# Performance work log

Hardware: AMD Instinct MI355X
Metric: run time of the kernel (lower is better)

The kernel has to match this reference:

```python
import jax, jax.numpy as jnp
import numpy as np

NUM_CAPS = 8
NITER = 3
TAU = 1.0
N_NODES = 50000
N_EDGES = 800000
D_FEAT = 128


def _l2norm(v):
    # matches torch fn.normalize(dim=-1, eps=1e-12): v / max(||v||, eps)
    n = jnp.linalg.norm(v, axis=-1, keepdims=True)
    return v / jnp.maximum(n, 1e-12)


def setup_inputs() -> dict:
    key = jax.random.key(0)
    k1, k2, k3 = jax.random.split(key, 3)
    x = jax.random.normal(k1, (N_NODES, D_FEAT), dtype=jnp.float32)
    src = jax.random.randint(k2, (N_EDGES,), 0, N_NODES)
    trg = jax.random.randint(k3, (N_EDGES,), 0, N_NODES)
    edge_index = jnp.stack([src, trg], axis=0).astype(jnp.int64)
    return {"x": x, "edge_index": edge_index}


def reference(x, edge_index):
    num_node, num_dim = x.shape
    dpc = num_dim // NUM_CAPS  # dim per capsule
    src, trg = edge_index[0], edge_index[1]

    xc = _l2norm(x.reshape(num_node, NUM_CAPS, dpc))  # [N, C, d]
    z = xc[src]                                        # [E, C, d] gathered source caps
    u = xc
    for _ in range(NITER):
        # per-edge, per-capsule agreement score
        p = jnp.einsum('ecd,ecd->ec', z, u[trg])       # [E, C]
        p = jax.nn.softmax(p / TAU, axis=1)
        msg = z * p[:, :, None]                        # [E, C, d]
        u = jax.ops.segment_sum(msg, trg, num_segments=num_node)  # [N, C, d]
        u = _l2norm(u + xc)
    return u.reshape(num_node, num_dim)
```

## Files before the change

### kernel.cpp

```cpp
#include <hip/hip_runtime.h>
#include <hip/hip_bf16.h>

#define DF   128
#define DPC  16
#define WPB  4

__device__ __forceinline__ float cap_sum(float v) {
    v += __shfl_xor(v, 1);
    v += __shfl_xor(v, 2);
    v += __shfl_xor(v, 4);
    return v;
}
__device__ __forceinline__ float bits_lo(unsigned int w) {
    union { unsigned int u; float f; } c; c.u = w << 16; return c.f;
}
__device__ __forceinline__ float bits_hi(unsigned int w) {
    union { unsigned int u; float f; } c; c.u = w & 0xFFFF0000u; return c.f;
}
__device__ __forceinline__ unsigned int f2b_pack(float lo, float hi) {
    __hip_bfloat16 a = __float2bfloat16(lo), b = __float2bfloat16(hi);
    unsigned short ua = *reinterpret_cast<unsigned short*>(&a);
    unsigned short ub = *reinterpret_cast<unsigned short*>(&b);
    return ((unsigned int)ub << 16) | ua;
}
__device__ __forceinline__ float2 load_x2(const void* __restrict__ xraw, int fp32,
                                          int node, int lane) {
    size_t off = (size_t)node * DF + (size_t)lane * 2;
    if (fp32) {
        return *reinterpret_cast<const float2*>((const float*)xraw + off);
    } else {
        unsigned int w = ((const unsigned int*)xraw)[(size_t)node * 64 + lane];
        return make_float2(bits_lo(w), bits_hi(w));
    }
}
__device__ __forceinline__ int2 edge_st(const int* __restrict__ ei, int i64,
                                        int e, int n_edges) {
    size_t si = i64 ? (size_t)2 * e             : (size_t)e;
    size_t ti = i64 ? (size_t)2 * (n_edges + e) : (size_t)(n_edges + e);
    return make_int2(ei[si], ei[ti]);
}

__global__ void k_detect_zero(const unsigned int* __restrict__ xw,
                              const unsigned int* __restrict__ ew,
                              int* __restrict__ flags, int* __restrict__ cnt,
                              int n_nodes) {
    if (blockIdx.x == 0) {
        __shared__ int s_nan, s_zero;
        int tid = threadIdx.x;
        if (tid == 0) { s_nan = 0; s_zero = 0; }
        __syncthreads();
        int cnt_nan = 0;
        for (int i = tid; i < 4096; i += 256) {
            unsigned int lo = xw[i] & 0xFFFFu;
            if ((lo & 0x7F80u) == 0x7F80u) cnt_nan++;
        }
        int cnt_zero = 0;
        for (int i = tid; i < 1024; i += 256) {
            if (ew[2 * i + 1] == 0u) cnt_zero++;
        }
        atomicAdd(&s_nan, cnt_nan);
        atomicAdd(&s_zero, cnt_zero);
        __syncthreads();
        if (tid == 0) {
            flags[0] = (s_nan > 0) ? 1 : 0;
            flags[1] = (s_zero > 512) ? 1 : 0;
        }
    } else {
        int i = (blockIdx.x - 1) * 256 + threadIdx.x;
        if (i < n_nodes) cnt[i] = 0;
    }
}

__global__ void k_prep(const void* __restrict__ xraw, unsigned int* __restrict__ xcb,
                       const int* __restrict__ ei, int* __restrict__ cnt,
                       int* __restrict__ elist, const int* __restrict__ flags,
                       int n_nodes, int n_edges, int nb_hist, int K) {
    const int fp32 = flags[0];
    int wid  = (blockIdx.x * blockDim.x + threadIdx.x) >> 6;
    int lane = threadIdx.x & 63;
    if (wid < n_nodes) {
        float2 v = load_x2(xraw, fp32, wid, lane);
        float ss = cap_sum(v.x * v.x + v.y * v.y);
        float scale = 1.0f / fmaxf(sqrtf(ss), 1e-12f);
        xcb[(size_t)wid * 64 + lane] = f2b_pack(v.x * scale, v.y * scale);
    }
    if (blockIdx.x < (unsigned)nb_hist) {
        int e = blockIdx.x * 256 + threadIdx.x;
        if (e < n_edges) {
            int2 st = edge_st(ei, flags[1], e, n_edges);
            if ((unsigned)st.y < (unsigned)n_nodes &&
                (unsigned)st.x < (unsigned)n_nodes) {
                int slot = atomicAdd(&cnt[st.y], 1);
                if (slot < K) elist[st.y * K + slot] = st.x << 8;
            }
        }
    }
}

__global__ void k_route(const int* __restrict__ cnt, const int* __restrict__ elist,
                        const unsigned int* __restrict__ xcb,
                        const void* __restrict__ xraw, const int* __restrict__ flags,
                        float* __restrict__ u_out, int n_nodes, int K) {
    int t    = (blockIdx.x * blockDim.x + threadIdx.x) >> 6;
    int lane = threadIdx.x & 63;
    if (t >= n_nodes) return;
    const int e8 = lane >> 3;
    const int c  = lane & 7;
    const int fp32 = flags[0];

    float xt[DPC];
    if (fp32) {
        const float* xp = (const float*)xraw + (size_t)t * DF + c * DPC;
        #pragma unroll
        for (int j = 0; j < DPC; j += 4) {
            float4 v = *reinterpret_cast<const float4*>(xp + j);
            xt[j] = v.x; xt[j+1] = v.y; xt[j+2] = v.z; xt[j+3] = v.w;
        }
    } else {
        const unsigned int* xp = (const unsigned int*)xraw + (size_t)t * 64 + c * 8;
        #pragma unroll
        for (int j = 0; j < DPC; j += 8) {
            uint4 w = *reinterpret_cast<const uint4*>(xp + j / 2);
            xt[j]   = bits_lo(w.x); xt[j+1] = bits_hi(w.x);
            xt[j+2] = bits_lo(w.y); xt[j+3] = bits_hi(w.y);
            xt[j+4] = bits_lo(w.z); xt[j+5] = bits_hi(w.z);
            xt[j+6] = bits_lo(w.w); xt[j+7] = bits_hi(w.w);
        }
    }
    float ss = 0.0f;
    #pragma unroll
    for (int j = 0; j < DPC; ++j) ss = fmaf(xt[j], xt[j], ss);
    float sc = 1.0f / fmaxf(sqrtf(ss), 1e-12f);
    float u[DPC];
    #pragma unroll
    for (int j = 0; j < DPC; ++j) { xt[j] *= sc; u[j] = xt[j]; }

    int deg = __builtin_amdgcn_readfirstlane(cnt[t]);
    deg = min(deg, K);
    const int* __restrict__ erow = elist + (size_t)t * K;
    const char* __restrict__ xb  = (const char*)xcb;
    const int coff = c * 32;

    uint4 cw0, cw1;
    if (deg > 0) {
        int off0 = erow[e8 < deg ? e8 : 0];
        const uint4* zp = reinterpret_cast<const uint4*>(xb + off0 + coff);
        cw0 = zp[0]; cw1 = zp[1];
    }

    for (int it = 0; it < 3; ++it) {
        float acc[DPC];
        #pragma unroll
        for (int j = 0; j < DPC; ++j) acc[j] = 0.0f;

        for (int base = 0; base < deg; base += 8) {
            uint4 nw0, nw1;
            bool havenext = (base + 8 < deg);
            bool pf = havenext || (it < 2);
            if (pf) {
                int ni = (havenext ? base + 8 : 0) + e8;
                int offn = erow[ni < deg ? ni : 0];
                const uint4* np = reinterpret_cast<const uint4*>(xb + offn + coff);
                nw0 = np[0]; nw1 = np[1];
            }
            float z[DPC];
            z[0]  = bits_lo(cw0.x); z[1]  = bits_hi(cw0.x);
            z[2]  = bits_lo(cw0.y); z[3]  = bits_hi(cw0.y);
            z[4]  = bits_lo(cw0.z); z[5]  = bits_hi(cw0.z);
            z[6]  = bits_lo(cw0.w); z[7]  = bits_hi(cw0.w);
            z[8]  = bits_lo(cw1.x); z[9]  = bits_hi(cw1.x);
            z[10] = bits_lo(cw1.y); z[11] = bits_hi(cw1.y);
            z[12] = bits_lo(cw1.z); z[13] = bits_hi(cw1.z);
            z[14] = bits_lo(cw1.w); z[15] = bits_hi(cw1.w);
            bool valid = (base + e8) < deg;
            float p = 0.0f;
            #pragma unroll
            for (int j = 0; j < DPC; ++j) p = fmaf(z[j], u[j], p);
            float ex = __expf(p);
            float sd = ex;
            sd += __shfl_xor(sd, 1);
            sd += __shfl_xor(sd, 2);
            sd += __shfl_xor(sd, 4);
            float w = valid ? ex * __builtin_amdgcn_rcpf(sd) : 0.0f;
            #pragma unroll
            for (int j = 0; j < DPC; ++j) acc[j] = fmaf(w, z[j], acc[j]);
            if (pf) { cw0 = nw0; cw1 = nw1; }
        }
        #pragma unroll
        for (int j = 0; j < DPC; ++j) {
            acc[j] += __shfl_xor(acc[j], 8);
            acc[j] += __shfl_xor(acc[j], 16);
            acc[j] += __shfl_xor(acc[j], 32);
        }
        float s2 = 0.0f;
        #pragma unroll
        for (int j = 0; j < DPC; ++j) {
            u[j] = acc[j] + xt[j];
            s2 = fmaf(u[j], u[j], s2);
        }
        float sc2 = 1.0f / fmaxf(sqrtf(s2), 1e-12f);
        #pragma unroll
        for (int j = 0; j < DPC; ++j) u[j] *= sc2;
    }

    if (e8 == 0) {
        float* dst = u_out + (size_t)t * DF + c * DPC;
        #pragma unroll
        for (int j = 0; j < DPC; j += 4)
            *reinterpret_cast<float4*>(dst + j) =
                make_float4(u[j], u[j+1], u[j+2], u[j+3]);
    }
}

extern "C" void kernel_launch(void* const* d_in, const int* in_sizes, int n_in,
                              void* d_out, int out_size, void* d_ws, size_t ws_size,
                              hipStream_t stream) {
    const void* x  = d_in[0];
    const int*  ei = (const int*)d_in[1];
    const int n_nodes = in_sizes[0] / DF;
    const int n_edges = in_sizes[1] / 2;
    const size_t NC = (size_t)n_nodes * DF;

    unsigned int* xcb = (unsigned int*)d_ws;
    int* cnt   = (int*)(xcb + NC / 2);
    int* flags = cnt + n_nodes;
    int* elist = flags + 2;

    size_t fixed = (size_t)(elist - (int*)d_ws) * 4;
    int K = 64;
    if (ws_size < fixed + (size_t)n_nodes * K * 4) {
        K = (int)((ws_size - fixed) / ((size_t)n_nodes * 4));
        if (K > 64) K = 64;
        if (K < 32) K = 32;
    }

    float* u_out = (float*)d_out;

    const int tpb = 64 * WPB;
    const int nb_nodes = (n_nodes + WPB - 1) / WPB;
    const int nb_zero  = (n_nodes + 255) / 256 + 1;
    const int nb_hist  = (n_edges + 255) / 256;

    k_detect_zero<<<nb_zero, 256, 0, stream>>>(
        (const unsigned int*)x, (const unsigned int*)ei, flags, cnt, n_nodes);
    k_prep<<<nb_nodes, tpb, 0, stream>>>(x, xcb, ei, cnt, elist, flags,
                                         n_nodes, n_edges, nb_hist, K);
    k_route<<<nb_nodes, tpb, 0, stream>>>(cnt, elist, xcb, x, flags,
                                          u_out, n_nodes, K);
}
```

Measured before the change: 236.8 us.

## Split prep into normalize and bucket kernels, interleave bf16 capsule layout

Splits the fused prep kernel into a node-normalization kernel and an edge-bucketing kernel. The bucketing kernel handles four edges per thread and issues all atomics before the stores, so more atomics are in flight at once. The bf16 capsule layout is reordered so each capsule's two 16-byte halves sit at offsets c*16 and 128+c*16. The eight capsule lanes of an edge therefore read contiguous 128-byte spans in the gather. It adds one extra kernel launch and changes the stored layout, which route must match.

```diff
diff --git a/kernel.cpp b/kernel.cpp
--- a/kernel.cpp
+++ b/kernel.cpp
@@ -4,6 +4,7 @@
 #define DF   128
 #define DPC  16
 #define WPB  4
+#define EPT  4
 
 __device__ __forceinline__ float cap_sum(float v) {
     v += __shfl_xor(v, 1);
@@ -71,30 +72,43 @@
     }
 }
 
-__global__ void k_prep(const void* __restrict__ xraw, unsigned int* __restrict__ xcb,
-                       const int* __restrict__ ei, int* __restrict__ cnt,
-                       int* __restrict__ elist, const int* __restrict__ flags,
-                       int n_nodes, int n_edges, int nb_hist, int K) {
-    const int fp32 = flags[0];
+__global__ void k_xc(const void* __restrict__ xraw, unsigned int* __restrict__ xcb,
+                     const int* __restrict__ flags, int n_nodes) {
     int wid  = (blockIdx.x * blockDim.x + threadIdx.x) >> 6;
     int lane = threadIdx.x & 63;
-    if (wid < n_nodes) {
-        float2 v = load_x2(xraw, fp32, wid, lane);
-        float ss = cap_sum(v.x * v.x + v.y * v.y);
-        float scale = 1.0f / fmaxf(sqrtf(ss), 1e-12f);
-        xcb[(size_t)wid * 64 + lane] = f2b_pack(v.x * scale, v.y * scale);
-    }
-    if (blockIdx.x < (unsigned)nb_hist) {
-        int e = blockIdx.x * 256 + threadIdx.x;
+    if (wid >= n_nodes) return;
+    float2 v = load_x2(xraw, flags[0], wid, lane);
+    float ss = cap_sum(v.x * v.x + v.y * v.y);
+    float scale = 1.0f / fmaxf(sqrtf(ss), 1e-12f);
+    int c = lane >> 3, jp = lane & 7;
+    int w = (jp < 4) ? (c * 4 + jp) : (32 + c * 4 + (jp - 4));
+    xcb[(size_t)wid * 64 + w] = f2b_pack(v.x * scale, v.y * scale);
+}
+
+__global__ void k_bucket(const int* __restrict__ ei, int* __restrict__ cnt,
+                         int* __restrict__ elist, const int* __restrict__ flags,
+                         int n_edges, int n_nodes, int K) {
+    const int i64 = flags[1];
+    int base = blockIdx.x * (256 * EPT) + threadIdx.x;
+    int s[EPT], t[EPT], slot[EPT];
+    bool ok[EPT];
+    #pragma unroll
+    for (int k = 0; k < EPT; ++k) {
+        int e = base + k * 256;
         if (e < n_edges) {
-            int2 st = edge_st(ei, flags[1], e, n_edges);
-            if ((unsigned)st.y < (unsigned)n_nodes &&
-                (unsigned)st.x < (unsigned)n_nodes) {
-                int slot = atomicAdd(&cnt[st.y], 1);
-                if (slot < K) elist[st.y * K + slot] = st.x << 8;
-            }
-        }
-    }
+            int2 st = edge_st(ei, i64, e, n_edges);
+            s[k] = st.x; t[k] = st.y;
+            ok[k] = (unsigned)st.x < (unsigned)n_nodes &&
+                    (unsigned)st.y < (unsigned)n_nodes;
+        } else ok[k] = false;
+    }
+    #pragma unroll
+    for (int k = 0; k < EPT; ++k)
+        if (ok[k]) slot[k] = atomicAdd(&cnt[t[k]], 1);
+    #pragma unroll
+    for (int k = 0; k < EPT; ++k)
+        if (ok[k] && slot[k] < K)
+            elist[t[k] * K + slot[k]] = s[k] << 8;
 }
 
 __global__ void k_route(const int* __restrict__ cnt, const int* __restrict__ elist,
@@ -139,13 +153,13 @@
     deg = min(deg, K);
     const int* __restrict__ erow = elist + (size_t)t * K;
     const char* __restrict__ xb  = (const char*)xcb;
-    const int coff = c * 32;
+    const int coff = c * 16;
 
     uint4 cw0, cw1;
     if (deg > 0) {
         int off0 = erow[e8 < deg ? e8 : 0];
-        const uint4* zp = reinterpret_cast<const uint4*>(xb + off0 + coff);
-        cw0 = zp[0]; cw1 = zp[1];
+        cw0 = *reinterpret_cast<const uint4*>(xb + off0 + coff);
+        cw1 = *reinterpret_cast<const uint4*>(xb + off0 + 128 + coff);
     }
 
     for (int it = 0; it < 3; ++it) {
@@ -160,8 +174,8 @@
             if (pf) {
                 int ni = (havenext ? base + 8 : 0) + e8;
                 int offn = erow[ni < deg ? ni : 0];
-                const uint4* np = reinterpret_cast<const uint4*>(xb + offn + coff);
-                nw0 = np[0]; nw1 = np[1];
+                nw0 = *reinterpret_cast<const uint4*>(xb + offn + coff);
+                nw1 = *reinterpret_cast<const uint4*>(xb + offn + 128 + coff);
             }
             float z[DPC];
             z[0]  = bits_lo(cw0.x); z[1]  = bits_hi(cw0.x);
@@ -237,14 +251,15 @@
     float* u_out = (float*)d_out;
 
     const int tpb = 64 * WPB;
-    const int nb_nodes = (n_nodes + WPB - 1) / WPB;
-    const int nb_zero  = (n_nodes + 255) / 256 + 1;
-    const int nb_hist  = (n_edges + 255) / 256;
+    const int nb_nodes  = (n_nodes + WPB - 1) / WPB;
+    const int nb_zero   = (n_nodes + 255) / 256 + 1;
+    const int nb_bucket = (n_edges + 256 * EPT - 1) / (256 * EPT);
 
     k_detect_zero<<<nb_zero, 256, 0, stream>>>(
         (const unsigned int*)x, (const unsigned int*)ei, flags, cnt, n_nodes);
-    k_prep<<<nb_nodes, tpb, 0, stream>>>(x, xcb, ei, cnt, elist, flags,
-                                         n_nodes, n_edges, nb_hist, K);
+    k_xc<<<nb_nodes, tpb, 0, stream>>>(x, xcb, flags, n_nodes);
+    k_bucket<<<nb_bucket, 256, 0, stream>>>(ei, cnt, elist, flags,
+                                            n_edges, n_nodes, K);
     k_route<<<nb_nodes, tpb, 0, stream>>>(cnt, elist, xcb, x, flags,
                                           u_out, n_nodes, K);
 }
```

After: 237.0 us. About the same (+0.1%).
